# Kernel tuning notes

Hardware: AMD Instinct MI355X
Metric: run time of the kernel (lower is better)

The kernel has to match this reference:

```python
import jax, jax.numpy as jnp
import numpy as np

# --- fan-beam geometry (matches init_kwargs geometry dict) ---
VOL = 256            # volume is VOL x VOL pixels
SPACING = 1.0        # volume pixel spacing (world units)
N_PROJ = 256         # number of projection angles
N_DET = 384          # detector pixel count
DET_SPACING = 1.2    # detector pixel spacing
ANG_RANGE = 2.0 * np.pi
SID = 400.0          # source-isocenter distance
SDD = 800.0          # source-detector distance
N_SAMPLES = 256      # samples along each ray (covers volume diagonal)


def _ray_sample_points():
    """World-space sample points along each (angle, detector-pixel) ray.
    Returns pts [P, D, S, 2] and the step length dt."""
    theta = jnp.arange(N_PROJ, dtype=jnp.float32) * (ANG_RANGE / N_PROJ)
    cen = jnp.stack([jnp.cos(theta), jnp.sin(theta)], axis=-1)     # central ray dir [P,2]
    u = jnp.stack([-jnp.sin(theta), jnp.cos(theta)], axis=-1)      # detector axis  [P,2]
    src = -SID * cen                                               # source position [P,2]
    det_off = (jnp.arange(N_DET, dtype=jnp.float32) - (N_DET - 1) / 2.0) * DET_SPACING
    # flat detector pixel positions [P,D,2]
    det = src[:, None, :] + SDD * cen[:, None, :] + det_off[None, :, None] * u[:, None, :]
    ray = det - src[:, None, :]
    ray = ray / jnp.linalg.norm(ray, axis=-1, keepdims=True)       # unit ray dirs [P,D,2]
    diag = SPACING * VOL * np.sqrt(2.0)                            # volume diagonal
    dt = jnp.float32(diag / N_SAMPLES)
    # sample the segment of each ray that can intersect the volume
    t = SID - diag / 2.0 + (jnp.arange(N_SAMPLES, dtype=jnp.float32) + 0.5) * dt  # [S]
    pts = src[:, None, None, :] + t[None, None, :, None] * ray[:, :, None, :]     # [P,D,S,2]
    return pts, dt


def _bilinear(img, pts):
    """Bilinear interpolation of img [H,W] at world points pts [...,2]; zero outside."""
    x = pts[..., 0] / SPACING + (VOL - 1) / 2.0   # fractional column index
    y = pts[..., 1] / SPACING + (VOL - 1) / 2.0   # fractional row index
    x0 = jnp.floor(x)
    y0 = jnp.floor(y)
    wx = x - x0
    y_w = y - y0
    x0i = x0.astype(jnp.int32)
    y0i = y0.astype(jnp.int32)

    def tap(yi, xi):
        inb = (xi >= 0) & (xi < VOL) & (yi >= 0) & (yi < VOL)
        v = img[jnp.clip(yi, 0, VOL - 1), jnp.clip(xi, 0, VOL - 1)]
        return jnp.where(inb, v, 0.0)

    return ((1 - wx) * (1 - y_w) * tap(y0i, x0i)
            + wx * (1 - y_w) * tap(y0i, x0i + 1)
            + (1 - wx) * y_w * tap(y0i + 1, x0i)
            + wx * y_w * tap(y0i + 1, x0i + 1))


def setup_inputs() -> dict:
    key = jax.random.key(0)
    x = jax.random.normal(key, (2, VOL, VOL, 1), dtype=jnp.float32)
    return {"x": x}


def reference(x):
    """Fan-beam forward projection: x [B,H,W,1] -> sinogram [B,P,D,1]."""
    pts, dt = _ray_sample_points()                 # [P,D,S,2], scalar

    def project_one(im):                           # im [H,W] -> sino [P,D]
        return _bilinear(im, pts).sum(axis=-1) * dt

    sino = jax.vmap(project_one)(x[..., 0])       # [B,P,D]
    return sino[..., None]                         # [B,P,D,1]
```

## Files before the change

### kernel.cpp

```cpp
#include <hip/hip_runtime.h>
#include <hip/hip_fp16.h>

#define NPROJ  256
#define NDET   384
#define NS     256
#define TW     258
#define TN     (TW * TW)
#define TPB    256

typedef _Float16 hvec2 __attribute__((ext_vector_type(2)));

__device__ __forceinline__ uint vp_pack(const float* im, int uy, int ux) {
    int x = ux - 1;
    if ((unsigned)x >= 256u) return 0u;
    float v0 = ((unsigned)(uy - 1) < 256u) ? im[((uy - 1) << 8) + x] : 0.0f;
    float v1 = ((unsigned)uy       < 256u) ? im[(uy << 8) + x]       : 0.0f;
    __half2 h2 = __floats2half2_rn(v0, v1);
    return *reinterpret_cast<uint*>(&h2);
}

__global__ void quad_build(const float* __restrict__ src, uint2* __restrict__ dst) {
    int idx = blockIdx.x * blockDim.x + threadIdx.x;
    if (idx >= 2 * TN) return;
    int b  = idx / TN;
    int e  = idx - b * TN;
    int uy = e / TW;
    int ux = e - uy * TW;
    const float* im = src + (b << 16);
    uint2 q;
    q.x = vp_pack(im, uy, ux);
    q.y = vp_pack(im, uy, ux + 1);
    dst[idx] = q;
}

__global__ __launch_bounds__(TPB) void fanproj_kernel(const uint2* __restrict__ Gq,
                                                      float* __restrict__ out) {
    int tid   = threadIdx.x;
    int lane  = tid & 63;
    int wv    = tid >> 6;
    int wray0 = (blockIdx.x << 5) + (wv << 3);
    int slot  = lane >> 3;
    int ray   = wray0 + (lane & 7);

    int d  = ray % NDET;
    int pb = ray / NDET;
    int p  = pb & (NPROJ - 1);
    int b  = pb >> 8;

    const float dt = 1.4142135623730951f;
    const float t0 = 219.68777079743137f;

    float theta = (float)p * (6.283185307179586f / (float)NPROJ);
    float st, ct;
    __sincosf(theta, &st, &ct);

    float srcx = -400.0f * ct;
    float srcy = -400.0f * st;
    float off  = ((float)d - 191.5f) * 1.2f;
    float rx   = fmaf(800.0f, ct, -off * st);
    float ry   = fmaf(800.0f, st,  off * ct);
    float n2   = rx * rx + ry * ry;
    float rn   = rsqrtf(n2);
    rn = rn * (1.5f - 0.5f * n2 * rn * rn);
    rx *= rn;
    ry *= rn;

    float bxu = fmaf(t0, rx, srcx) + 128.5f;
    float byu = fmaf(t0, ry, srcy) + 128.5f;
    float sx  = dt * rx;
    float sy  = dt * ry;

    const float EPS = 2e-3f;
    float sxs = (fabsf(sx) < 1e-9f) ? copysignf(1e-9f, sx) : sx;
    float sys = (fabsf(sy) < 1e-9f) ? copysignf(1e-9f, sy) : sy;
    float isx = 1.0f / sxs;
    float isy = 1.0f / sys;
    float ax0 = (0.0f - bxu) * isx, ax1 = (257.0f - bxu) * isx;
    float ay0 = (0.0f - byu) * isy, ay1 = (257.0f - byu) * isy;
    float lof = fmaxf(fminf(ax0, ax1), fminf(ay0, ay1)) + EPS;
    float hif = fminf(fmaxf(ax0, ax1), fmaxf(ay0, ay1)) - EPS;
    lof = fminf(fmaxf(lof, -1.0f), 300.0f);
    hif = fminf(fmaxf(hif, -1.0f), 300.0f);
    int slo = max(0,      (int)ceilf(lof));
    int shi = min(NS - 1, (int)floorf(hif));

    const uint2* Gb = Gq + (size_t)b * TN;

    float acc = 0.0f;
    float sf  = (float)(slo + slot);
    for (int s = slo + slot; s <= shi; s += 8) {
        float X = fmaf(sf, sx, bxu);
        float Y = fmaf(sf, sy, byu);
        sf += 8.0f;
        float xf = floorf(X);
        float yf = floorf(Y);
        float wx = X - xf;
        float wy = Y - yf;
        float aF = fmaf(yf, 258.0f, xf);
        aF = fminf(fmaxf(aF, 0.0f), 66563.0f);
        int ai = (int)aF;
        uint2 q = Gb[ai];
        hvec2 hw = __builtin_bit_cast(hvec2,
                       __builtin_amdgcn_cvt_pkrtz(1.0f - wy, wy));
        float c0 = __builtin_amdgcn_fdot2(__builtin_bit_cast(hvec2, q.x),
                                          hw, 0.0f, false);
        float c1 = __builtin_amdgcn_fdot2(__builtin_bit_cast(hvec2, q.y),
                                          hw, 0.0f, false);
        acc = fmaf(wx, c1 - c0, acc + c0);
    }

    acc += __shfl_xor(acc, 8,  64);
    acc += __shfl_xor(acc, 16, 64);
    acc += __shfl_xor(acc, 32, 64);
    if (slot == 0) out[ray] = acc * dt;
}

extern "C" void kernel_launch(void* const* d_in, const int* in_sizes, int n_in,
                              void* d_out, int out_size, void* d_ws, size_t ws_size,
                              hipStream_t stream) {
    const float* x = (const float*)d_in[0];
    float* out     = (float*)d_out;
    uint2* Gq      = (uint2*)d_ws;

    int nent = 2 * TN;
    quad_build<<<(nent + 255) / 256, 256, 0, stream>>>(x, Gq);

    fanproj_kernel<<<6144, TPB, 0, stream>>>(Gq, out);
}
```

Measured before the change: 81.85 us.

## Interleave both batch images in one table and process both per ray

After: 75.03 us. 8.3% less time.

```diff
diff --git a/kernel.cpp b/kernel.cpp
--- a/kernel.cpp
+++ b/kernel.cpp
@@ -6,6 +6,7 @@
 #define NS     256
 #define TW     258
 #define TN     (TW * TW)
+#define NRAY   (NPROJ * NDET)
 #define TPB    256
 
 typedef _Float16 hvec2 __attribute__((ext_vector_type(2)));
@@ -19,33 +20,32 @@
     return *reinterpret_cast<uint*>(&h2);
 }
 
-__global__ void quad_build(const float* __restrict__ src, uint2* __restrict__ dst) {
-    int idx = blockIdx.x * blockDim.x + threadIdx.x;
-    if (idx >= 2 * TN) return;
-    int b  = idx / TN;
-    int e  = idx - b * TN;
+__global__ void quad_build(const float* __restrict__ src, uint4* __restrict__ dst) {
+    int e = blockIdx.x * blockDim.x + threadIdx.x;
+    if (e >= TN) return;
     int uy = e / TW;
     int ux = e - uy * TW;
-    const float* im = src + (b << 16);
-    uint2 q;
-    q.x = vp_pack(im, uy, ux);
-    q.y = vp_pack(im, uy, ux + 1);
-    dst[idx] = q;
+    const float* im0 = src;
+    const float* im1 = src + (1 << 16);
+    uint4 q;
+    q.x = vp_pack(im0, uy, ux);
+    q.y = vp_pack(im0, uy, ux + 1);
+    q.z = vp_pack(im1, uy, ux);
+    q.w = vp_pack(im1, uy, ux + 1);
+    dst[e] = q;
 }
 
-__global__ __launch_bounds__(TPB) void fanproj_kernel(const uint2* __restrict__ Gq,
+__global__ __launch_bounds__(TPB) void fanproj_kernel(const uint4* __restrict__ T,
                                                       float* __restrict__ out) {
     int tid   = threadIdx.x;
     int lane  = tid & 63;
     int wv    = tid >> 6;
-    int wray0 = (blockIdx.x << 5) + (wv << 3);
+    int wrp0  = (blockIdx.x << 5) + (wv << 3);
     int slot  = lane >> 3;
-    int ray   = wray0 + (lane & 7);
+    int rp    = wrp0 + (lane & 7);
 
-    int d  = ray % NDET;
-    int pb = ray / NDET;
-    int p  = pb & (NPROJ - 1);
-    int b  = pb >> 8;
+    int d = rp % NDET;
+    int p = rp / NDET;
 
     const float dt = 1.4142135623730951f;
     const float t0 = 219.68777079743137f;
@@ -84,9 +84,7 @@
     int slo = max(0,      (int)ceilf(lof));
     int shi = min(NS - 1, (int)floorf(hif));
 
-    const uint2* Gb = Gq + (size_t)b * TN;
-
-    float acc = 0.0f;
+    float acc0 = 0.0f, acc1 = 0.0f;
     float sf  = (float)(slo + slot);
     for (int s = slo + slot; s <= shi; s += 8) {
         float X = fmaf(sf, sx, bxu);
@@ -99,20 +97,31 @@
         float aF = fmaf(yf, 258.0f, xf);
         aF = fminf(fmaxf(aF, 0.0f), 66563.0f);
         int ai = (int)aF;
-        uint2 q = Gb[ai];
+        uint4 q = T[ai];
         hvec2 hw = __builtin_bit_cast(hvec2,
                        __builtin_amdgcn_cvt_pkrtz(1.0f - wy, wy));
         float c0 = __builtin_amdgcn_fdot2(__builtin_bit_cast(hvec2, q.x),
                                           hw, 0.0f, false);
         float c1 = __builtin_amdgcn_fdot2(__builtin_bit_cast(hvec2, q.y),
                                           hw, 0.0f, false);
-        acc = fmaf(wx, c1 - c0, acc + c0);
+        acc0 = fmaf(wx, c1 - c0, acc0 + c0);
+        float c2 = __builtin_amdgcn_fdot2(__builtin_bit_cast(hvec2, q.z),
+                                          hw, 0.0f, false);
+        float c3 = __builtin_amdgcn_fdot2(__builtin_bit_cast(hvec2, q.w),
+                                          hw, 0.0f, false);
+        acc1 = fmaf(wx, c3 - c2, acc1 + c2);
     }
 
-    acc += __shfl_xor(acc, 8,  64);
-    acc += __shfl_xor(acc, 16, 64);
-    acc += __shfl_xor(acc, 32, 64);
-    if (slot == 0) out[ray] = acc * dt;
+    acc0 += __shfl_xor(acc0, 8,  64);
+    acc0 += __shfl_xor(acc0, 16, 64);
+    acc0 += __shfl_xor(acc0, 32, 64);
+    acc1 += __shfl_xor(acc1, 8,  64);
+    acc1 += __shfl_xor(acc1, 16, 64);
+    acc1 += __shfl_xor(acc1, 32, 64);
+    if (slot == 0) {
+        out[rp]        = acc0 * dt;
+        out[rp + NRAY] = acc1 * dt;
+    }
 }
 
 extern "C" void kernel_launch(void* const* d_in, const int* in_sizes, int n_in,
@@ -120,10 +129,9 @@
                               hipStream_t stream) {
     const float* x = (const float*)d_in[0];
     float* out     = (float*)d_out;
-    uint2* Gq      = (uint2*)d_ws;
+    uint4* T       = (uint4*)d_ws;
 
-    int nent = 2 * TN;
-    quad_build<<<(nent + 255) / 256, 256, 0, stream>>>(x, Gq);
+    quad_build<<<(TN + 255) / 256, 256, 0, stream>>>(x, T);
 
-    fanproj_kernel<<<6144, TPB, 0, stream>>>(Gq, out);
+    fanproj_kernel<<<3072, TPB, 0, stream>>>(T, out);
 }
```
